# Performance work log

Measured on AMD Instinct MI355X. Metric: run time of the kernel, lower is better.

## Reference

```python
import jax, jax.numpy as jnp
import numpy as np

D_MODEL = 256
D_HID = 128
EPS = 1e-5
MASK_VALUE = -10000.0


def _layer_norm(x, scale, bias):
    mu = jnp.mean(x, axis=-1, keepdims=True)
    var = jnp.mean(jnp.square(x - mu), axis=-1, keepdims=True)
    return (x - mu) * jax.lax.rsqrt(var + EPS) * scale + bias


def setup_inputs() -> dict:
    key = jax.random.key(0)
    ks = jax.random.split(key, 8)
    B, S = 32, 1024
    std = 0.02
    return {
        "x": jax.random.normal(ks[0], (B, S, D_MODEL), dtype=jnp.float32),
        "ln1_scale": jnp.ones((D_MODEL,), jnp.float32),
        "ln1_bias": jnp.zeros((D_MODEL,), jnp.float32),
        "w_qkv": jax.random.normal(ks[1], (D_MODEL, 3 * D_MODEL), jnp.float32) * std,
        "b_qkv": jnp.zeros((3 * D_MODEL,), jnp.float32),
        "w_proj": jax.random.normal(ks[2], (D_MODEL, D_MODEL), jnp.float32) * std,
        "b_proj": jnp.zeros((D_MODEL,), jnp.float32),
        "ln2_scale": jnp.ones((D_MODEL,), jnp.float32),
        "ln2_bias": jnp.zeros((D_MODEL,), jnp.float32),
        "w_fc1": jax.random.normal(ks[3], (D_MODEL, D_HID), jnp.float32) * std,
        "b_fc1": jnp.zeros((D_HID,), jnp.float32),
        "w_fc2": jax.random.normal(ks[4], (D_HID, D_MODEL), jnp.float32) * std,
        "b_fc2": jnp.zeros((D_MODEL,), jnp.float32),
    }


def reference(x, ln1_scale, ln1_bias, w_qkv, b_qkv, w_proj, b_proj,
              ln2_scale, ln2_bias, w_fc1, b_fc1, w_fc2, b_fc2):
    B, S, D = x.shape
    # --- pre-LN self-attention ---
    residual = x
    h = _layer_norm(x, ln1_scale, ln1_bias)
    qkv = h @ w_qkv + b_qkv                       # [B, S, 3D]
    q, k, v = jnp.split(qkv, 3, axis=2)           # each [B, S, D]; 1 head, head_dim=D
    scale = 1.0 / jnp.sqrt(jnp.asarray(D, x.dtype))
    scores = jnp.einsum('bqd,bkd->bqk', q, k) * scale   # [B, S, S]
    causal = jnp.tril(jnp.ones((S, S), dtype=bool))
    scores = jnp.where(causal[None, :, :], scores, MASK_VALUE)
    attn = jax.nn.softmax(scores, axis=-1)        # dropout is identity (eval mode)
    out = jnp.einsum('bqk,bkd->bqd', attn, v)     # [B, S, D]
    out = out @ w_proj + b_proj
    x = out + residual
    # --- pre-LN MLP ---
    residual = x
    h = _layer_norm(x, ln2_scale, ln2_bias)
    h = jax.nn.relu(h @ w_fc1 + b_fc1)
    h = h @ w_fc2 + b_fc2
    return h + residual
```

## Files before the change

### kernel.cpp

```cpp
#include <hip/hip_runtime.h>
#include <hip/hip_bf16.h>

#define D_MODEL 256
#define D_HID   128
#define SEQ     1024
#define NBATCH  32
#define NROWS   (NBATCH * SEQ)
#define MASKV   -10000.0f
#define EPSLN   1e-5f

typedef unsigned short u16;
using bf16x8 = __attribute__((ext_vector_type(8))) short;
using f32x4  = __attribute__((ext_vector_type(4))) float;

union U8 { uint4 v; u16 s[8]; };

__device__ __forceinline__ float bf2f(u16 u) {
    unsigned int x = ((unsigned int)u) << 16;
    return __uint_as_float(x);
}
__device__ __forceinline__ u16 f2bf(float f) {
    unsigned int u = __float_as_uint(f);
    u += 0x7fff + ((u >> 16) & 1);
    return (u16)(u >> 16);
}
__device__ __forceinline__ void load4(const float* p, float* f) {
    float4 a = *(const float4*)p;
    f[0] = a.x; f[1] = a.y; f[2] = a.z; f[3] = a.w;
}
__device__ __forceinline__ void load4(const u16* p, float* f) {
    ushort4 v = *(const ushort4*)p;
    f[0] = bf2f(v.x); f[1] = bf2f(v.y); f[2] = bf2f(v.z); f[3] = bf2f(v.w);
}
__device__ __forceinline__ void gload16(const u16* g, u16* l) {
    __builtin_amdgcn_global_load_lds(
        (const __attribute__((address_space(1))) void*)g,
        (__attribute__((address_space(3))) void*)l, 16, 0, 0);
}

template <int CTRL>
__device__ __forceinline__ float dpp_mov(float v) {
    return __int_as_float(__builtin_amdgcn_update_dpp(
        0, __float_as_int(v), CTRL, 0xf, 0xf, true));
}
__device__ __forceinline__ float red16_max(float v) {
    v = fmaxf(v, dpp_mov<0xB1>(v));
    v = fmaxf(v, dpp_mov<0x4E>(v));
    v = fmaxf(v, dpp_mov<0x141>(v));
    v = fmaxf(v, dpp_mov<0x140>(v));
    return v;
}
__device__ __forceinline__ float red16_sum(float v) {
    v += dpp_mov<0xB1>(v);
    v += dpp_mov<0x4E>(v);
    v += dpp_mov<0x141>(v);
    v += dpp_mov<0x140>(v);
    return v;
}

__global__ __launch_bounds__(256) void transpose_weights(
    const float* __restrict__ wqkv, u16* __restrict__ wqkvT,
    const float* __restrict__ wproj, u16* __restrict__ wprojT,
    const float* __restrict__ wfc1, u16* __restrict__ wfc1T,
    const float* __restrict__ wfc2, u16* __restrict__ wfc2T) {
    int tid = blockIdx.x * 256 + threadIdx.x;
    int stride = gridDim.x * 256;
    for (int i = tid; i < 768 * 256; i += stride) {
        int n = i >> 8, k = i & 255;
        wqkvT[i] = f2bf(wqkv[k * 768 + n]);
    }
    for (int i = tid; i < 256 * 256; i += stride) {
        int n = i >> 8, k = i & 255;
        wprojT[i] = f2bf(wproj[k * 256 + n]);
    }
    for (int i = tid; i < 128 * 256; i += stride) {
        int n = i >> 8, k = i & 255;
        wfc1T[i] = f2bf(wfc1[k * 128 + n]);
    }
    for (int i = tid; i < 256 * 128; i += stride) {
        int n = i >> 7, k = i & 127;
        wfc2T[i] = f2bf(wfc2[k * 256 + n]);
    }
}

template <typename TX>
__global__ __launch_bounds__(256) void ln_fused(
    const TX* __restrict__ x, const float* __restrict__ gamma,
    const float* __restrict__ beta, u16* __restrict__ out) {
    int wave = threadIdx.x >> 6, lane = threadIdx.x & 63;
    int row = blockIdx.x * 4 + wave;
    float f[4];
    load4(x + (size_t)row * D_MODEL + lane * 4, f);
    float s  = f[0] + f[1] + f[2] + f[3];
    float sq = f[0] * f[0] + f[1] * f[1] + f[2] * f[2] + f[3] * f[3];
    #pragma unroll
    for (int off = 1; off < 64; off <<= 1) {
        s  += __shfl_xor(s, off);
        sq += __shfl_xor(sq, off);
    }
    float mu   = s * (1.0f / 256.0f);
    float var  = sq * (1.0f / 256.0f) - mu * mu;
    float rstd = rsqrtf(var + EPSLN);
    float g[4], be[4];
    load4(gamma + lane * 4, g);
    load4(beta + lane * 4, be);
    ushort4 o;
    o.x = f2bf((f[0] - mu) * rstd * g[0] + be[0]);
    o.y = f2bf((f[1] - mu) * rstd * g[1] + be[1]);
    o.z = f2bf((f[2] - mu) * rstd * g[2] + be[2]);
    o.w = f2bf((f[3] - mu) * rstd * g[3] + be[3]);
    *(ushort4*)(out + (size_t)row * D_MODEL + lane * 4) = o;
}

#define GT2_ELEMS (2 * 128 * 128)

template <int K>
__device__ __forceinline__ void gemm_tile2(
    const u16* __restrict__ A, const u16* __restrict__ BT,
    int m0, int n0, u16* lds, f32x4 acc[4][4]) {
    u16* ldsA = lds;
    u16* ldsB = lds + 128 * 128;
    const int tid = threadIdx.x;
    const int lane = tid & 63, wave = tid >> 6;
    const int wr = (wave >> 1) * 64, wc = (wave & 1) * 64;
    const int row = lane & 15, quad = lane >> 4;

    for (int ks = 0; ks < K; ks += 128) {
        __syncthreads();
        #pragma unroll
        for (int i = 0; i < 8; i++) {
            int blk = i * 4 + wave;
            int B = (blk << 10) + lane * 16;
            int r = B >> 8;
            int cb = (B & 255) ^ ((r & 7) << 4);
            gload16(A + (size_t)(m0 + r) * K + ks + (cb >> 1),
                    ldsA + (blk << 9));
            gload16(BT + (size_t)(n0 + r) * K + ks + (cb >> 1),
                    ldsB + (blk << 9));
        }
        __syncthreads();
        #pragma unroll
        for (int k0 = 0; k0 < 128; k0 += 32) {
            bf16x8 a[4], b[4];
            #pragma unroll
            for (int mi = 0; mi < 4; mi++) {
                int rr = wr + mi * 16 + row;
                a[mi] = *(const bf16x8*)(ldsA + rr * 128 +
                         ((k0 + quad * 8) ^ ((rr & 7) << 3)));
            }
            #pragma unroll
            for (int nj = 0; nj < 4; nj++) {
                int rr = wc + nj * 16 + row;
                b[nj] = *(const bf16x8*)(ldsB + rr * 128 +
                         ((k0 + quad * 8) ^ ((rr & 7) << 3)));
            }
            #pragma unroll
            for (int mi = 0; mi < 4; mi++)
                #pragma unroll
                for (int nj = 0; nj < 4; nj++)
                    acc[mi][nj] = __builtin_amdgcn_mfma_f32_16x16x32_bf16(
                        a[mi], b[nj], acc[mi][nj], 0, 0, 0);
        }
    }
}

#define ZERO_ACC4(acc)                                       \
    _Pragma("unroll") for (int i_ = 0; i_ < 4; i_++)         \
    _Pragma("unroll") for (int j_ = 0; j_ < 4; j_++)         \
    _Pragma("unroll") for (int e_ = 0; e_ < 4; e_++) acc[i_][j_][e_] = 0.0f;

#define EPILOG_IDX4                                          \
    int lane = threadIdx.x & 63, wave = threadIdx.x >> 6;    \
    int wr = (wave >> 1) * 64, wc = (wave & 1) * 64;         \
    int row = lane & 15, quad = lane >> 4;

__global__ __launch_bounds__(256) void gemm_qkv(
    const u16* __restrict__ h, const u16* __restrict__ wqkvT,
    const float* __restrict__ b_qkv,
    u16* __restrict__ q, u16* __restrict__ kk, u16* __restrict__ vT) {
    __shared__ u16 lds[GT2_ELEMS];
    f32x4 acc[4][4];
    ZERO_ACC4(acc)
    int m0 = blockIdx.x * 128, n0 = blockIdx.y * 128;
    gemm_tile2<256>(h, wqkvT, m0, n0, lds, acc);
    EPILOG_IDX4
    #pragma unroll
    for (int mi = 0; mi < 4; mi++) {
        #pragma unroll
        for (int nj = 0; nj < 4; nj++) {
            int gn = n0 + wc + nj * 16 + row;
            float bias = b_qkv[gn];
            int gm = m0 + wr + mi * 16 + quad * 4;
            if (gn < 256) {
                #pragma unroll
                for (int r = 0; r < 4; r++)
                    q[(size_t)(gm + r) * 256 + gn] =
                        f2bf((acc[mi][nj][r] + bias) * 0.0625f);
            } else if (gn < 512) {
                int col = gn - 256;
                #pragma unroll
                for (int r = 0; r < 4; r++)
                    kk[(size_t)(gm + r) * 256 + col] = f2bf(acc[mi][nj][r] + bias);
            } else {
                int d = gn - 512;
                int b = gm >> 10, s = gm & 1023;
                ushort4 pack;
                pack.x = f2bf(acc[mi][nj][0] + bias);
                pack.y = f2bf(acc[mi][nj][1] + bias);
                pack.z = f2bf(acc[mi][nj][2] + bias);
                pack.w = f2bf(acc[mi][nj][3] + bias);
                *(ushort4*)(vT + ((size_t)(b * 256 + d) << 10) + s) = pack;
            }
        }
    }
}

__global__ __launch_bounds__(256) void gemm_proj(
    const u16* __restrict__ ao, const u16* __restrict__ wprojT,
    const float* __restrict__ b_proj, const float* __restrict__ x_in,
    u16* __restrict__ x2) {
    __shared__ u16 lds[GT2_ELEMS];
    f32x4 acc[4][4];
    ZERO_ACC4(acc)
    int m0 = blockIdx.x * 128, n0 = blockIdx.y * 128;
    gemm_tile2<256>(ao, wprojT, m0, n0, lds, acc);
    EPILOG_IDX4
    #pragma unroll
    for (int mi = 0; mi < 4; mi++)
        #pragma unroll
        for (int nj = 0; nj < 4; nj++) {
            int gn = n0 + wc + nj * 16 + row;
            float bias = b_proj[gn];
            int gm = m0 + wr + mi * 16 + quad * 4;
            #pragma unroll
            for (int r = 0; r < 4; r++) {
                size_t idx = (size_t)(gm + r) * 256 + gn;
                x2[idx] = f2bf(acc[mi][nj][r] + bias + x_in[idx]);
            }
        }
}

__global__ __launch_bounds__(256) void gemm_mlp(
    const u16* __restrict__ x2, const float* __restrict__ g2,
    const float* __restrict__ be2,
    const u16* __restrict__ wfc1T, const float* __restrict__ b_fc1,
    const u16* __restrict__ wfc2T, const float* __restrict__ b_fc2,
    float* __restrict__ out) {
    __shared__ u16 lds[65536];
    u16* ldsB1 = lds + 32768;
    u16* ldsA1 = lds + 49152;
    const int tid = threadIdx.x;
    const int lane = tid & 63, wave = tid >> 6;
    const int rowl = lane & 15, quad = lane >> 4;
    const int wr = (wave >> 1) * 64, wc = (wave & 1) * 64;
    const int m0 = blockIdx.x * 128;

    #pragma unroll
    for (int i = 0; i < 16; i++) {
        int blk = i * 4 + wave;
        int B = (blk << 10) + lane * 16;
        int r = B >> 9;
        int cb = (B & 511) ^ ((r & 7) << 4);
        gload16(x2 + (size_t)(m0 + r) * 256 + (cb >> 1), lds + (B >> 1));
    }
    #pragma unroll
    for (int i = 0; i < 8; i++) {
        int blk = i * 4 + wave;
        int B = (blk << 10) + lane * 16;
        int r = B >> 8;
        int cb = (B & 255) ^ ((r & 7) << 4);
        gload16(wfc1T + (size_t)r * 256 + 0 + (cb >> 1), ldsB1 + (B >> 1));
    }
    __syncthreads();

    {
        float4 g4  = *(const float4*)(g2 + lane * 4);
        float4 be4 = *(const float4*)(be2 + lane * 4);
        #pragma unroll 4
        for (int i = 0; i < 32; i++) {
            int r = wave + i * 4;
            char* p = (char*)lds + r * 512 + ((lane * 8) ^ ((r & 7) << 4));
            ushort4 v = *(ushort4*)p;
            float f0 = bf2f(v.x), f1 = bf2f(v.y), f2v = bf2f(v.z), f3 = bf2f(v.w);
            float s  = f0 + f1 + f2v + f3;
            float sq = f0*f0 + f1*f1 + f2v*f2v + f3*f3;
            s = red16_sum(s);   s += __shfl_xor(s, 16);   s += __shfl_xor(s, 32);
            sq = red16_sum(sq); sq += __shfl_xor(sq, 16); sq += __shfl_xor(sq, 32);
            float mu   = s * (1.0f / 256.0f);
            float var  = sq * (1.0f / 256.0f) - mu * mu;
            float rstd = rsqrtf(var + EPSLN);
            ushort4 o;
            o.x = f2bf((f0  - mu) * rstd * g4.x + be4.x);
            o.y = f2bf((f1  - mu) * rstd * g4.y + be4.y);
            o.z = f2bf((f2v - mu) * rstd * g4.z + be4.z);
            o.w = f2bf((f3  - mu) * rstd * g4.w + be4.w);
            *(ushort4*)p = o;
        }
    }
    __syncthreads();

    f32x4 acc1[4][4];
    ZERO_ACC4(acc1)
    #pragma unroll
    for (int ks = 0; ks < 256; ks += 128) {
        if (ks) {
            __syncthreads();
            #pragma unroll
            for (int i = 0; i < 8; i++) {
                int blk = i * 4 + wave;
                int B = (blk << 10) + lane * 16;
                int r = B >> 8;
                int cb = (B & 255) ^ ((r & 7) << 4);
                gload16(wfc1T + (size_t)r * 256 + ks + (cb >> 1),
                        ldsB1 + (B >> 1));
            }
            __syncthreads();
        }
        #pragma unroll
        for (int k0 = 0; k0 < 128; k0 += 32) {
            bf16x8 a[4], b[4];
            #pragma unroll
            for (int mi = 0; mi < 4; mi++) {
                int rr = wr + mi * 16 + rowl;
                a[mi] = *(const bf16x8*)((const char*)lds + rr * 512 +
                         ((((ks + k0 + quad * 8) << 1)) ^ ((rr & 7) << 4)));
            }
            #pragma unroll
            for (int nj = 0; nj < 4; nj++) {
                int rb = wc + nj * 16 + rowl;
                b[nj] = *(const bf16x8*)((const char*)ldsB1 + rb * 256 +
                         ((((k0 + quad * 8) << 1)) ^ ((rb & 7) << 4)));
            }
            #pragma unroll
            for (int mi = 0; mi < 4; mi++)
                #pragma unroll
                for (int nj = 0; nj < 4; nj++)
                    acc1[mi][nj] = __builtin_amdgcn_mfma_f32_16x16x32_bf16(
                        a[mi], b[nj], acc1[mi][nj], 0, 0, 0);
        }
    }
    #pragma unroll
    for (int mi = 0; mi < 4; mi++)
        #pragma unroll
        for (int nj = 0; nj < 4; nj++) {
            int gn_l = wc + nj * 16 + rowl;
            float bias = b_fc1[gn_l];
            #pragma unroll
            for (int r = 0; r < 4; r++) {
                int gm_l = wr + mi * 16 + quad * 4 + r;
                *(u16*)((char*)ldsA1 + gm_l * 256 +
                        (((gn_l << 1)) ^ ((gm_l & 7) << 4))) =
                    f2bf(fmaxf(acc1[mi][nj][r] + bias, 0.0f));
            }
        }
    __syncthreads();

    #pragma unroll
    for (int i = 0; i < 16; i++) {
        int blk = i * 4 + wave;
        int B = (blk << 10) + lane * 16;
        int r = B >> 8;
        int cb = (B & 255) ^ ((r & 7) << 4);
        gload16(wfc2T + (size_t)r * 128 + (cb >> 1), lds + (B >> 1));
    }
    __syncthreads();

    const int wc2 = (wave & 1) * 128;
    f32x4 acc2[4][8];
    #pragma unroll
    for (int mi = 0; mi < 4; mi++)
        #pragma unroll
        for (int nj = 0; nj < 8; nj++)
            #pragma unroll
            for (int e = 0; e < 4; e++) acc2[mi][nj][e] = 0.0f;
    #pragma unroll
    for (int k0 = 0; k0 < 128; k0 += 32) {
        bf16x8 a[4], b[8];
        #pragma unroll
        for (int mi = 0; mi < 4; mi++) {
            int rr = wr + mi * 16 + rowl;
            a[mi] = *(const bf16x8*)((const char*)ldsA1 + rr * 256 +
                     ((((k0 + quad * 8) << 1)) ^ ((rr & 7) << 4)));
        }
        #pragma unroll
        for (int nj = 0; nj < 8; nj++) {
            int rb = wc2 + nj * 16 + rowl;
            b[nj] = *(const bf16x8*)((const char*)lds + rb * 256 +
                     ((((k0 + quad * 8) << 1)) ^ ((rb & 7) << 4)));
        }
        #pragma unroll
        for (int mi = 0; mi < 4; mi++)
            #pragma unroll
            for (int nj = 0; nj < 8; nj++)
                acc2[mi][nj] = __builtin_amdgcn_mfma_f32_16x16x32_bf16(
                    a[mi], b[nj], acc2[mi][nj], 0, 0, 0);
    }
    #pragma unroll
    for (int mi = 0; mi < 4; mi++)
        #pragma unroll
        for (int nj = 0; nj < 8; nj++) {
            int gn = wc2 + nj * 16 + rowl;
            float bias = b_fc2[gn];
            int gm = m0 + wr + mi * 16 + quad * 4;
            #pragma unroll
            for (int r = 0; r < 4; r++) {
                size_t idx = (size_t)(gm + r) * 256 + gn;
                out[idx] = acc2[mi][nj][r] + bias + bf2f(x2[idx]);
            }
        }
}

__constant__ unsigned char CQT[15] = {7,6,6,5,5,4,4,7, 0,1,1,2,2,3,3};
__constant__ unsigned char CH[15]  = {0,0,1,0,1,0,1,1, 2,0,1,0,1,0,1};

__global__ __launch_bounds__(512) void attn_kernel(
    const u16* __restrict__ q, const u16* __restrict__ k,
    const u16* __restrict__ vT, u16* __restrict__ ao,
    u16* __restrict__ part, float* __restrict__ ml) {
    __shared__ u16 k_lds[2][32 * 256];
    __shared__ u16 v_lds[2][256 * 32];
    __shared__ u16 p_lds[8][16 * 40];

    int j = blockIdx.x;
    int b = j & 31, c = j >> 5;
    int qt = CQT[c], ch = CH[c];
    int span = 2 * qt + 2;
    int lo, hi;
    if (ch == 2) { lo = 0; hi = 4; }
    else         { lo = ch * span; hi = lo + span; }

    int tid = threadIdx.x;
    int lane = tid & 63, wave = tid >> 6;
    int row = lane & 15, quad = lane >> 4;
    int qrow0 = qt * 128 + wave * 16;

    const u16* qb = q + ((size_t)b << 10) * 256;
    const u16* kb = k + ((size_t)b << 10) * 256;
    const u16* vb = vT + (((size_t)b * 256) << 10);

    const int kxor = (row & 7) << 3;
    const int vxor = (row & 6) << 2;

    bf16x8 qf[8];
    #pragma unroll
    for (int kf = 0; kf < 8; kf++)
        qf[kf] = *(const bf16x8*)(qb + (size_t)(qrow0 + row) * 256 + kf * 32 + quad * 8);

    f32x4 o[16];
    #pragma unroll
    for (int n = 0; n < 16; n++)
        #pragma unroll
        for (int e = 0; e < 4; e++) o[n][e] = 0.0f;
    float m_i[4], l_i[4];
    #pragma unroll
    for (int r = 0; r < 4; r++) { m_i[r] = -1e30f; l_i[r] = 0.0f; }

    int wlast = 4 * qt + (wave >> 1);

    auto stage = [&](int bf, int kt) {
        int k0 = kt << 5;
        #pragma unroll
        for (int cc = 0; cc < 2; cc++) {
            int blk = wave * 2 + cc;
            int B = (blk << 10) + lane * 16;
            int rk = B >> 9;
            int ck = (B & 511) ^ ((rk & 7) << 4);
            gload16(kb + (size_t)(k0 + rk) * 256 + (ck >> 1),
                    &k_lds[bf][blk << 9]);
            int rv = B >> 6;
            int cv = (B & 63) ^ ((rv & 6) << 3);
            gload16(vb + ((size_t)rv << 10) + k0 + (cv >> 1),
                    &v_lds[bf][blk << 9]);
        }
    };

    stage(0, lo);
    __syncthreads();

    for (int kt = lo; kt < hi; kt++) {
        int cur = (kt - lo) & 1;
        if (kt + 1 < hi) stage(cur ^ 1, kt + 1);
        if (kt <= wlast) {
            const u16* kl = k_lds[cur];
            const u16* vl = v_lds[cur];

            f32x4 sf[2];
            #pragma unroll
            for (int jn = 0; jn < 2; jn++)
                #pragma unroll
                for (int e = 0; e < 4; e++) sf[jn][e] = 0.0f;
            __builtin_amdgcn_s_setprio(1);
            #pragma unroll
            for (int kf = 0; kf < 8; kf++)
                #pragma unroll
                for (int jn = 0; jn < 2; jn++) {
                    bf16x8 bfrag = *(const bf16x8*)(kl +
                        ((((jn * 16 + row) * 256) + kf * 32 + quad * 8) ^ kxor));
                    sf[jn] = __builtin_amdgcn_mfma_f32_16x16x32_bf16(
                        qf[kf], bfrag, sf[jn], 0, 0, 0);
                }
            __builtin_amdgcn_s_setprio(0);

            int kk0 = kt * 32;
            bool diag = (kt == wlast);
            int qrow = qrow0 + quad * 4;
            float sv[2][4];
            #pragma unroll
            for (int jn = 0; jn < 2; jn++)
                #pragma unroll
                for (int r = 0; r < 4; r++) {
                    float v = sf[jn][r];
                    if (diag && (kk0 + jn * 16 + row > qrow + r)) v = MASKV;
                    sv[jn][r] = v;
                }

            float pmax[4];
            int need = 0;
            #pragma unroll
            for (int r = 0; r < 4; r++) {
                pmax[r] = red16_max(fmaxf(sv[0][r], sv[1][r]));
                need |= (pmax[r] > m_i[r] + 8.0f) ? 1 : 0;
            }
            if (__any(need)) {
                #pragma unroll
                for (int r = 0; r < 4; r++) {
                    float mnew = fmaxf(m_i[r], pmax[r]);
                    float al = __expf(m_i[r] - mnew);
                    m_i[r] = mnew;
                    l_i[r] *= al;
                    #pragma unroll
                    for (int n = 0; n < 16; n++) o[n][r] *= al;
                }
            }
            #pragma unroll
            for (int r = 0; r < 4; r++) {
                float ps = 0.0f;
                #pragma unroll
                for (int jn = 0; jn < 2; jn++) {
                    sv[jn][r] = __expf(sv[jn][r] - m_i[r]);
                    ps += sv[jn][r];
                }
                l_i[r] += red16_sum(ps);
            }

            u16* pw = p_lds[wave];
            #pragma unroll
            for (int jn = 0; jn < 2; jn++)
                #pragma unroll
                for (int r = 0; r < 4; r++)
                    pw[(quad * 4 + r) * 40 + jn * 16 + row] = f2bf(sv[jn][r]);
            bf16x8 pf = *(const bf16x8*)(pw + row * 40 + quad * 8);

            __builtin_amdgcn_s_setprio(1);
            #pragma unroll
            for (int n = 0; n < 16; n++) {
                bf16x8 bv = *(const bf16x8*)(vl +
                    ((((n * 16 + row) * 32) + quad * 8) ^ vxor));
                o[n] = __builtin_amdgcn_mfma_f32_16x16x32_bf16(pf, bv, o[n], 0, 0, 0);
            }
            __builtin_amdgcn_s_setprio(0);
        }
        __syncthreads();
    }

    if (ch == 2) {
        float inv[4];
        #pragma unroll
        for (int r = 0; r < 4; r++) inv[r] = 1.0f / l_i[r];
        u16* aob = ao + (((size_t)b << 10) + qrow0) * 256;
        #pragma unroll
        for (int r = 0; r < 4; r++)
            #pragma unroll
            for (int n = 0; n < 16; n++)
                aob[(size_t)(quad * 4 + r) * 256 + n * 16 + row] =
                    f2bf(o[n][r] * inv[r]);
    } else {
        int pq = b * 7 + (qt - 1);
        u16* pb = part + ((size_t)(ch * 224 + pq) << 15);
        #pragma unroll
        for (int r = 0; r < 4; r++) {
            int rt = wave * 16 + quad * 4 + r;
            #pragma unroll
            for (int n = 0; n < 16; n++)
                pb[(size_t)rt * 256 + n * 16 + row] = f2bf(o[n][r]);
        }
        if (row == 0) {
            int p = pq * 2 + ch;
            #pragma unroll
            for (int r = 0; r < 4; r++) {
                int rt = wave * 16 + quad * 4 + r;
                float2 v2; v2.x = m_i[r]; v2.y = l_i[r];
                *(float2*)(ml + ((size_t)(p * 128 + rt)) * 2) = v2;
            }
        }
    }
}

__global__ __launch_bounds__(256) void attn_merge(
    const u16* __restrict__ part, const float* __restrict__ ml,
    u16* __restrict__ ao) {
    int j = blockIdx.x;
    int b = j / 14, rem = j - b * 14;
    int qt = (rem >> 1) + 1, rh = rem & 1;
    int t = threadIdx.x;
    int r = t >> 2, cq = t & 3;
    int rt = rh * 64 + r;
    int pq = b * 7 + (qt - 1);
    const float* mlA = ml + ((size_t)((pq * 2 + 0) * 128 + rt)) * 2;
    const float* mlB = ml + ((size_t)((pq * 2 + 1) * 128 + rt)) * 2;
    float mA = mlA[0], lA = mlA[1];
    float mB = mlB[0], lB = mlB[1];
    float m  = fmaxf(mA, mB);
    float eA = __expf(mA - m), eB = __expf(mB - m);
    float inv = 1.0f / (lA * eA + lB * eB);
    float sA = eA * inv, sB = eB * inv;
    const u16* oA = part + ((size_t)pq << 15) + (size_t)rt * 256 + cq * 64;
    const u16* oB = part + ((size_t)(224 + pq) << 15) + (size_t)rt * 256 + cq * 64;
    u16* dst = ao + ((size_t)((b << 10) + qt * 128 + rt)) * 256 + cq * 64;
    #pragma unroll
    for (int u = 0; u < 8; u++) {
        U8 a, bb, o;
        a.v  = *(const uint4*)(oA + u * 8);
        bb.v = *(const uint4*)(oB + u * 8);
        #pragma unroll
        for (int e = 0; e < 8; e++)
            o.s[e] = f2bf(bf2f(a.s[e]) * sA + bf2f(bb.s[e]) * sB);
        *(uint4*)(dst + u * 8) = o.v;
    }
}

extern "C" void kernel_launch(void* const* d_in, const int* in_sizes, int n_in,
                              void* d_out, int out_size, void* d_ws, size_t ws_size,
                              hipStream_t stream) {
    const float* x      = (const float*)d_in[0];
    const float* ln1_s  = (const float*)d_in[1];
    const float* ln1_b  = (const float*)d_in[2];
    const float* w_qkv  = (const float*)d_in[3];
    const float* b_qkv  = (const float*)d_in[4];
    const float* w_proj = (const float*)d_in[5];
    const float* b_proj = (const float*)d_in[6];
    const float* ln2_s  = (const float*)d_in[7];
    const float* ln2_b  = (const float*)d_in[8];
    const float* w_fc1  = (const float*)d_in[9];
    const float* b_fc1  = (const float*)d_in[10];
    const float* w_fc2  = (const float*)d_in[11];
    const float* b_fc2  = (const float*)d_in[12];
    float* out = (float*)d_out;

    u16* h = (u16*)d_out;

    u16* W = (u16*)d_ws;
    u16* wqkvT  = W;
    u16* wprojT = wqkvT + 196608;
    u16* wfc1T  = wprojT + 65536;
    u16* wfc2T  = wfc1T + 32768;
    u16* buf1   = wfc2T + 32768;
    u16* buf2   = buf1 + (size_t)NROWS * 256;
    u16* buf3   = buf2 + (size_t)NROWS * 256;

    u16*   part  = h;
    float* mlbuf = (float*)d_out + 7340032;

    transpose_weights<<<dim3(64), dim3(256), 0, stream>>>(
        w_qkv, wqkvT, w_proj, wprojT, w_fc1, wfc1T, w_fc2, wfc2T);
    ln_fused<float><<<dim3(NROWS / 4), dim3(256), 0, stream>>>(
        x, ln1_s, ln1_b, h);
    gemm_qkv<<<dim3(NROWS / 128, 6), dim3(256), 0, stream>>>(
        h, wqkvT, b_qkv, buf1, buf2, buf3);
    attn_kernel<<<dim3(480), dim3(512), 0, stream>>>(
        buf1, buf2, buf3, buf1, part, mlbuf);
    attn_merge<<<dim3(448), dim3(256), 0, stream>>>(
        part, mlbuf, buf1);
    gemm_proj<<<dim3(NROWS / 128, 2), dim3(256), 0, stream>>>(
        buf1, wprojT, b_proj, x, buf2);
    gemm_mlp<<<dim3(NROWS / 128), dim3(256), 0, stream>>>(
        buf2, ln2_s, ln2_b, wfc1T, b_fc1, wfc2T, b_fc2, out);
}
```

Measured before the change: 244.2 us.

## Fuse attention split merge into proj GEMM, merge prep kernels, widen MLP blocks

Three changes. The weight transpose and LN1 kernels become a single launch. The split-KV attention merge now runs inside the projection GEMM, which combines the two partial outputs as it loads the A tile into LDS, so the separate merge kernel and its write and reread of the attention output go away. The MLP kernel moves to 512 threads with 8 waves, each handling half as many rows, to lower registers per wave and raise parallelism, at the cost of partial outputs being reread by both N-blocks of the proj GEMM and A-tile loads now going through registers instead of async LDS loads.

New measurement: 227.4 us. -6.9%, faster.

```diff
diff --git a/kernel.cpp b/kernel.cpp
--- a/kernel.cpp
+++ b/kernel.cpp
@@ -28,10 +28,6 @@
     float4 a = *(const float4*)p;
     f[0] = a.x; f[1] = a.y; f[2] = a.z; f[3] = a.w;
 }
-__device__ __forceinline__ void load4(const u16* p, float* f) {
-    ushort4 v = *(const ushort4*)p;
-    f[0] = bf2f(v.x); f[1] = bf2f(v.y); f[2] = bf2f(v.z); f[3] = bf2f(v.w);
-}
 __device__ __forceinline__ void gload16(const u16* g, u16* l) {
     __builtin_amdgcn_global_load_lds(
         (const __attribute__((address_space(1))) void*)g,
@@ -58,58 +54,57 @@
     return v;
 }
 
-__global__ __launch_bounds__(256) void transpose_weights(
+__global__ __launch_bounds__(256) void prep_kernel(
     const float* __restrict__ wqkv, u16* __restrict__ wqkvT,
     const float* __restrict__ wproj, u16* __restrict__ wprojT,
     const float* __restrict__ wfc1, u16* __restrict__ wfc1T,
-    const float* __restrict__ wfc2, u16* __restrict__ wfc2T) {
-    int tid = blockIdx.x * 256 + threadIdx.x;
-    int stride = gridDim.x * 256;
-    for (int i = tid; i < 768 * 256; i += stride) {
-        int n = i >> 8, k = i & 255;
-        wqkvT[i] = f2bf(wqkv[k * 768 + n]);
-    }
-    for (int i = tid; i < 256 * 256; i += stride) {
-        int n = i >> 8, k = i & 255;
-        wprojT[i] = f2bf(wproj[k * 256 + n]);
-    }
-    for (int i = tid; i < 128 * 256; i += stride) {
-        int n = i >> 8, k = i & 255;
-        wfc1T[i] = f2bf(wfc1[k * 128 + n]);
-    }
-    for (int i = tid; i < 256 * 128; i += stride) {
-        int n = i >> 7, k = i & 127;
-        wfc2T[i] = f2bf(wfc2[k * 256 + n]);
-    }
-}
-
-template <typename TX>
-__global__ __launch_bounds__(256) void ln_fused(
-    const TX* __restrict__ x, const float* __restrict__ gamma,
-    const float* __restrict__ beta, u16* __restrict__ out) {
-    int wave = threadIdx.x >> 6, lane = threadIdx.x & 63;
-    int row = blockIdx.x * 4 + wave;
-    float f[4];
-    load4(x + (size_t)row * D_MODEL + lane * 4, f);
-    float s  = f[0] + f[1] + f[2] + f[3];
-    float sq = f[0] * f[0] + f[1] * f[1] + f[2] * f[2] + f[3] * f[3];
-    #pragma unroll
-    for (int off = 1; off < 64; off <<= 1) {
-        s  += __shfl_xor(s, off);
-        sq += __shfl_xor(sq, off);
-    }
-    float mu   = s * (1.0f / 256.0f);
-    float var  = sq * (1.0f / 256.0f) - mu * mu;
-    float rstd = rsqrtf(var + EPSLN);
-    float g[4], be[4];
-    load4(gamma + lane * 4, g);
-    load4(beta + lane * 4, be);
-    ushort4 o;
-    o.x = f2bf((f[0] - mu) * rstd * g[0] + be[0]);
-    o.y = f2bf((f[1] - mu) * rstd * g[1] + be[1]);
-    o.z = f2bf((f[2] - mu) * rstd * g[2] + be[2]);
-    o.w = f2bf((f[3] - mu) * rstd * g[3] + be[3]);
-    *(ushort4*)(out + (size_t)row * D_MODEL + lane * 4) = o;
+    const float* __restrict__ wfc2, u16* __restrict__ wfc2T,
+    const float* __restrict__ x, const float* __restrict__ g1,
+    const float* __restrict__ be1, u16* __restrict__ h) {
+    if (blockIdx.x < 64) {
+        int tid = blockIdx.x * 256 + threadIdx.x;
+        const int stride = 64 * 256;
+        for (int i = tid; i < 768 * 256; i += stride) {
+            int n = i >> 8, k = i & 255;
+            wqkvT[i] = f2bf(wqkv[k * 768 + n]);
+        }
+        for (int i = tid; i < 256 * 256; i += stride) {
+            int n = i >> 8, k = i & 255;
+            wprojT[i] = f2bf(wproj[k * 256 + n]);
+        }
+        for (int i = tid; i < 128 * 256; i += stride) {
+            int n = i >> 8, k = i & 255;
+            wfc1T[i] = f2bf(wfc1[k * 128 + n]);
+        }
+        for (int i = tid; i < 256 * 128; i += stride) {
+            int n = i >> 7, k = i & 127;
+            wfc2T[i] = f2bf(wfc2[k * 256 + n]);
+        }
+    } else {
+        int wave = threadIdx.x >> 6, lane = threadIdx.x & 63;
+        int row = (blockIdx.x - 64) * 4 + wave;
+        float f[4];
+        load4(x + (size_t)row * D_MODEL + lane * 4, f);
+        float s  = f[0] + f[1] + f[2] + f[3];
+        float sq = f[0] * f[0] + f[1] * f[1] + f[2] * f[2] + f[3] * f[3];
+        #pragma unroll
+        for (int off = 1; off < 64; off <<= 1) {
+            s  += __shfl_xor(s, off);
+            sq += __shfl_xor(sq, off);
+        }
+        float mu   = s * (1.0f / 256.0f);
+        float var  = sq * (1.0f / 256.0f) - mu * mu;
+        float rstd = rsqrtf(var + EPSLN);
+        float g[4], be[4];
+        load4(g1 + lane * 4, g);
+        load4(be1 + lane * 4, be);
+        ushort4 o;
+        o.x = f2bf((f[0] - mu) * rstd * g[0] + be[0]);
+        o.y = f2bf((f[1] - mu) * rstd * g[1] + be[1]);
+        o.z = f2bf((f[2] - mu) * rstd * g[2] + be[2]);
+        o.w = f2bf((f[3] - mu) * rstd * g[3] + be[3]);
+        *(ushort4*)(h + (size_t)row * D_MODEL + lane * 4) = o;
+    }
 }
 
 #define GT2_ELEMS (2 * 128 * 128)
@@ -215,16 +210,102 @@
     }
 }
 
-__global__ __launch_bounds__(256) void gemm_proj(
-    const u16* __restrict__ ao, const u16* __restrict__ wprojT,
+__global__ __launch_bounds__(256) void gemm_proj_m(
+    const u16* __restrict__ part, const float* __restrict__ ml,
+    const u16* __restrict__ aoq0, const u16* __restrict__ wprojT,
     const float* __restrict__ b_proj, const float* __restrict__ x_in,
     u16* __restrict__ x2) {
     __shared__ u16 lds[GT2_ELEMS];
+    __shared__ float s_sc[2][128];
+    u16* ldsA = lds;
+    u16* ldsB = lds + 128 * 128;
+    const int tid = threadIdx.x;
+    const int lane = tid & 63, wave = tid >> 6;
+    const int wr = (wave >> 1) * 64, wc = (wave & 1) * 64;
+    const int row = lane & 15, quad = lane >> 4;
+    int m0 = blockIdx.x * 128, n0 = blockIdx.y * 128;
+    int b = m0 >> 10, qt = (m0 >> 7) & 7;
+    int pq = b * 7 + qt - 1;
+
+    if (qt && tid < 128) {
+        const float* pA = ml + ((size_t)((pq * 2 + 0) * 128 + tid)) * 2;
+        const float* pB = ml + ((size_t)((pq * 2 + 1) * 128 + tid)) * 2;
+        float mA = pA[0], lA = pA[1];
+        float mB = pB[0], lB = pB[1];
+        float m  = fmaxf(mA, mB);
+        float eA = __expf(mA - m), eB = __expf(mB - m);
+        float inv = 1.0f / (lA * eA + lB * eB);
+        s_sc[0][tid] = eA * inv;
+        s_sc[1][tid] = eB * inv;
+    }
+
     f32x4 acc[4][4];
     ZERO_ACC4(acc)
-    int m0 = blockIdx.x * 128, n0 = blockIdx.y * 128;
-    gemm_tile2<256>(ao, wprojT, m0, n0, lds, acc);
-    EPILOG_IDX4
+    for (int ks = 0; ks < 256; ks += 128) {
+        __syncthreads();
+        if (qt == 0) {
+            #pragma unroll
+            for (int i = 0; i < 8; i++) {
+                int blk = i * 4 + wave;
+                int B = (blk << 10) + lane * 16;
+                int r = B >> 8;
+                int cb = (B & 255) ^ ((r & 7) << 4);
+                gload16(aoq0 + (size_t)(m0 + r) * 256 + ks + (cb >> 1),
+                        ldsA + (blk << 9));
+                gload16(wprojT + (size_t)(n0 + r) * 256 + ks + (cb >> 1),
+                        ldsB + (blk << 9));
+            }
+        } else {
+            #pragma unroll
+            for (int i = 0; i < 8; i++) {
+                int blk = i * 4 + wave;
+                int B = (blk << 10) + lane * 16;
+                int r = B >> 8;
+                int cb = (B & 255) ^ ((r & 7) << 4);
+                gload16(wprojT + (size_t)(n0 + r) * 256 + ks + (cb >> 1),
+                        ldsB + (blk << 9));
+            }
+            const u16* p0 = part + ((size_t)pq << 15);
+            const u16* p1 = part + ((size_t)(224 + pq) << 15);
+            #pragma unroll
+            for (int i = 0; i < 8; i++) {
+                int cchunk = i * 256 + tid;
+                int Bb = cchunk * 16;
+                int r = Bb >> 8, cb_lin = Bb & 255;
+                U8 a, bb, o;
+                a.v  = *(const uint4*)(p0 + (size_t)r * 256 + ks + (cb_lin >> 1));
+                bb.v = *(const uint4*)(p1 + (size_t)r * 256 + ks + (cb_lin >> 1));
+                float sA = s_sc[0][r], sB = s_sc[1][r];
+                #pragma unroll
+                for (int e = 0; e < 8; e++)
+                    o.s[e] = f2bf(bf2f(a.s[e]) * sA + bf2f(bb.s[e]) * sB);
+                *(uint4*)((char*)ldsA + r * 256 + (cb_lin ^ ((r & 7) << 4))) = o.v;
+            }
+        }
+        __syncthreads();
+        #pragma unroll
+        for (int k0 = 0; k0 < 128; k0 += 32) {
+            bf16x8 a[4], bfr[4];
+            #pragma unroll
+            for (int mi = 0; mi < 4; mi++) {
+                int rr = wr + mi * 16 + row;
+                a[mi] = *(const bf16x8*)(ldsA + rr * 128 +
+                         ((k0 + quad * 8) ^ ((rr & 7) << 3)));
+            }
+            #pragma unroll
+            for (int nj = 0; nj < 4; nj++) {
+                int rr = wc + nj * 16 + row;
+                bfr[nj] = *(const bf16x8*)(ldsB + rr * 128 +
+                         ((k0 + quad * 8) ^ ((rr & 7) << 3)));
+            }
+            #pragma unroll
+            for (int mi = 0; mi < 4; mi++)
+                #pragma unroll
+                for (int nj = 0; nj < 4; nj++)
+                    acc[mi][nj] = __builtin_amdgcn_mfma_f32_16x16x32_bf16(
+                        a[mi], bfr[nj], acc[mi][nj], 0, 0, 0);
+        }
+    }
     #pragma unroll
     for (int mi = 0; mi < 4; mi++)
         #pragma unroll
@@ -240,7 +321,7 @@
         }
 }
 
-__global__ __launch_bounds__(256) void gemm_mlp(
+__global__ __launch_bounds__(512) void gemm_mlp(
     const u16* __restrict__ x2, const float* __restrict__ g2,
     const float* __restrict__ be2,
     const u16* __restrict__ wfc1T, const float* __restrict__ b_fc1,
@@ -252,20 +333,20 @@
     const int tid = threadIdx.x;
     const int lane = tid & 63, wave = tid >> 6;
     const int rowl = lane & 15, quad = lane >> 4;
-    const int wr = (wave >> 1) * 64, wc = (wave & 1) * 64;
+    const int wr = (wave >> 1) * 32, wc = (wave & 1) * 64;
     const int m0 = blockIdx.x * 128;
 
     #pragma unroll
-    for (int i = 0; i < 16; i++) {
-        int blk = i * 4 + wave;
+    for (int i = 0; i < 8; i++) {
+        int blk = i * 8 + wave;
         int B = (blk << 10) + lane * 16;
         int r = B >> 9;
         int cb = (B & 511) ^ ((r & 7) << 4);
         gload16(x2 + (size_t)(m0 + r) * 256 + (cb >> 1), lds + (B >> 1));
     }
     #pragma unroll
-    for (int i = 0; i < 8; i++) {
-        int blk = i * 4 + wave;
+    for (int i = 0; i < 4; i++) {
+        int blk = i * 8 + wave;
         int B = (blk << 10) + lane * 16;
         int r = B >> 8;
         int cb = (B & 255) ^ ((r & 7) << 4);
@@ -277,8 +358,8 @@
         float4 g4  = *(const float4*)(g2 + lane * 4);
         float4 be4 = *(const float4*)(be2 + lane * 4);
         #pragma unroll 4
-        for (int i = 0; i < 32; i++) {
-            int r = wave + i * 4;
+        for (int i = 0; i < 16; i++) {
+            int r = wave + i * 8;
             char* p = (char*)lds + r * 512 + ((lane * 8) ^ ((r & 7) << 4));
             ushort4 v = *(ushort4*)p;
             float f0 = bf2f(v.x), f1 = bf2f(v.y), f2v = bf2f(v.z), f3 = bf2f(v.w);
@@ -299,15 +380,20 @@
     }
     __syncthreads();
 
-    f32x4 acc1[4][4];
-    ZERO_ACC4(acc1)
+    f32x4 acc1[2][4];
+    #pragma unroll
+    for (int mi = 0; mi < 2; mi++)
+        #pragma unroll
+        for (int nj = 0; nj < 4; nj++)
+            #pragma unroll
+            for (int e = 0; e < 4; e++) acc1[mi][nj][e] = 0.0f;
     #pragma unroll
     for (int ks = 0; ks < 256; ks += 128) {
         if (ks) {
             __syncthreads();
             #pragma unroll
-            for (int i = 0; i < 8; i++) {
-                int blk = i * 4 + wave;
+            for (int i = 0; i < 4; i++) {
+                int blk = i * 8 + wave;
                 int B = (blk << 10) + lane * 16;
                 int r = B >> 8;
                 int cb = (B & 255) ^ ((r & 7) << 4);
@@ -318,9 +404,9 @@
         }
         #pragma unroll
         for (int k0 = 0; k0 < 128; k0 += 32) {
-            bf16x8 a[4], b[4];
-            #pragma unroll
-            for (int mi = 0; mi < 4; mi++) {
+            bf16x8 a[2], b[4];
+            #pragma unroll
+            for (int mi = 0; mi < 2; mi++) {
                 int rr = wr + mi * 16 + rowl;
                 a[mi] = *(const bf16x8*)((const char*)lds + rr * 512 +
                          ((((ks + k0 + quad * 8) << 1)) ^ ((rr & 7) << 4)));
@@ -332,7 +418,7 @@
                          ((((k0 + quad * 8) << 1)) ^ ((rb & 7) << 4)));
             }
             #pragma unroll
-            for (int mi = 0; mi < 4; mi++)
+            for (int mi = 0; mi < 2; mi++)
                 #pragma unroll
                 for (int nj = 0; nj < 4; nj++)
                     acc1[mi][nj] = __builtin_amdgcn_mfma_f32_16x16x32_bf16(
@@ -340,7 +426,7 @@
         }
     }
     #pragma unroll
-    for (int mi = 0; mi < 4; mi++)
+    for (int mi = 0; mi < 2; mi++)
         #pragma unroll
         for (int nj = 0; nj < 4; nj++) {
             int gn_l = wc + nj * 16 + rowl;
@@ -356,8 +442,8 @@
     __syncthreads();
 
     #pragma unroll
-    for (int i = 0; i < 16; i++) {
-        int blk = i * 4 + wave;
+    for (int i = 0; i < 8; i++) {
+        int blk = i * 8 + wave;
         int B = (blk << 10) + lane * 16;
         int r = B >> 8;
         int cb = (B & 255) ^ ((r & 7) << 4);
@@ -366,18 +452,18 @@
     __syncthreads();
 
     const int wc2 = (wave & 1) * 128;
-    f32x4 acc2[4][8];
-    #pragma unroll
-    for (int mi = 0; mi < 4; mi++)
+    f32x4 acc2[2][8];
+    #pragma unroll
+    for (int mi = 0; mi < 2; mi++)
         #pragma unroll
         for (int nj = 0; nj < 8; nj++)
             #pragma unroll
             for (int e = 0; e < 4; e++) acc2[mi][nj][e] = 0.0f;
     #pragma unroll
     for (int k0 = 0; k0 < 128; k0 += 32) {
-        bf16x8 a[4], b[8];
-        #pragma unroll
-        for (int mi = 0; mi < 4; mi++) {
+        bf16x8 a[2], b[8];
+        #pragma unroll
+        for (int mi = 0; mi < 2; mi++) {
             int rr = wr + mi * 16 + rowl;
             a[mi] = *(const bf16x8*)((const char*)ldsA1 + rr * 256 +
                      ((((k0 + quad * 8) << 1)) ^ ((rr & 7) << 4)));
@@ -389,14 +475,14 @@
                      ((((k0 + quad * 8) << 1)) ^ ((rb & 7) << 4)));
         }
         #pragma unroll
-        for (int mi = 0; mi < 4; mi++)
+        for (int mi = 0; mi < 2; mi++)
             #pragma unroll
             for (int nj = 0; nj < 8; nj++)
                 acc2[mi][nj] = __builtin_amdgcn_mfma_f32_16x16x32_bf16(
                     a[mi], b[nj], acc2[mi][nj], 0, 0, 0);
     }
     #pragma unroll
-    for (int mi = 0; mi < 4; mi++)
+    for (int mi = 0; mi < 2; mi++)
         #pragma unroll
         for (int nj = 0; nj < 8; nj++) {
             int gn = wc2 + nj * 16 + rowl;
@@ -593,39 +679,6 @@
                 *(float2*)(ml + ((size_t)(p * 128 + rt)) * 2) = v2;
             }
         }
-    }
-}
-
-__global__ __launch_bounds__(256) void attn_merge(
-    const u16* __restrict__ part, const float* __restrict__ ml,
-    u16* __restrict__ ao) {
-    int j = blockIdx.x;
-    int b = j / 14, rem = j - b * 14;
-    int qt = (rem >> 1) + 1, rh = rem & 1;
-    int t = threadIdx.x;
-    int r = t >> 2, cq = t & 3;
-    int rt = rh * 64 + r;
-    int pq = b * 7 + (qt - 1);
-    const float* mlA = ml + ((size_t)((pq * 2 + 0) * 128 + rt)) * 2;
-    const float* mlB = ml + ((size_t)((pq * 2 + 1) * 128 + rt)) * 2;
-    float mA = mlA[0], lA = mlA[1];
-    float mB = mlB[0], lB = mlB[1];
-    float m  = fmaxf(mA, mB);
-    float eA = __expf(mA - m), eB = __expf(mB - m);
-    float inv = 1.0f / (lA * eA + lB * eB);
-    float sA = eA * inv, sB = eB * inv;
-    const u16* oA = part + ((size_t)pq << 15) + (size_t)rt * 256 + cq * 64;
-    const u16* oB = part + ((size_t)(224 + pq) << 15) + (size_t)rt * 256 + cq * 64;
-    u16* dst = ao + ((size_t)((b << 10) + qt * 128 + rt)) * 256 + cq * 64;
-    #pragma unroll
-    for (int u = 0; u < 8; u++) {
-        U8 a, bb, o;
-        a.v  = *(const uint4*)(oA + u * 8);
-        bb.v = *(const uint4*)(oB + u * 8);
-        #pragma unroll
-        for (int e = 0; e < 8; e++)
-            o.s[e] = f2bf(bf2f(a.s[e]) * sA + bf2f(bb.s[e]) * sB);
-        *(uint4*)(dst + u * 8) = o.v;
     }
 }
 
@@ -661,18 +714,15 @@
     u16*   part  = h;
     float* mlbuf = (float*)d_out + 7340032;
 
-    transpose_weights<<<dim3(64), dim3(256), 0, stream>>>(
-        w_qkv, wqkvT, w_proj, wprojT, w_fc1, wfc1T, w_fc2, wfc2T);
-    ln_fused<float><<<dim3(NROWS / 4), dim3(256), 0, stream>>>(
+    prep_kernel<<<dim3(64 + NROWS / 4), dim3(256), 0, stream>>>(
+        w_qkv, wqkvT, w_proj, wprojT, w_fc1, wfc1T, w_fc2, wfc2T,
         x, ln1_s, ln1_b, h);
     gemm_qkv<<<dim3(NROWS / 128, 6), dim3(256), 0, stream>>>(
         h, wqkvT, b_qkv, buf1, buf2, buf3);
     attn_kernel<<<dim3(480), dim3(512), 0, stream>>>(
         buf1, buf2, buf3, buf1, part, mlbuf);
-    attn_merge<<<dim3(448), dim3(256), 0, stream>>>(
-        part, mlbuf, buf1);
-    gemm_proj<<<dim3(NROWS / 128, 2), dim3(256), 0, stream>>>(
-        buf1, wprojT, b_proj, x, buf2);
-    gemm_mlp<<<dim3(NROWS / 128), dim3(256), 0, stream>>>(
+    gemm_proj_m<<<dim3(NROWS / 128, 2), dim3(256), 0, stream>>>(
+        part, mlbuf, buf1, wprojT, b_proj, x, buf2);
+    gemm_mlp<<<dim3(NROWS / 128), dim3(512), 0, stream>>>(
         buf2, ln2_s, ln2_b, wfc1T, b_fc1, wfc2T, b_fc2, out);
 }
```
